# Performance work log

Measured on AMD Instinct MI355X. Metric: run time of the kernel, lower is better.

## Reference

```python
import jax, jax.numpy as jnp
import numpy as np

B, C, H, W = 8, 1, 256, 256
ALPHA, GAMMA = 0.25, 2.0
DICE_W, BOUNDARY_W, FOCAL_W = 1.0, 0.5, 1.0
EPS = 1e-06


def _dt1d(f, axis):
    # exact 1D squared-distance transform: out[i] = min_j (i-j)^2 + f[j]
    n = f.shape[axis]
    f = jnp.moveaxis(f, axis, -1)
    i = jnp.arange(n)
    D = ((i[:, None] - i[None, :]) ** 2).astype(f.dtype)  # [n, n]
    out = jnp.min(f[..., None, :] + D, axis=-1)
    return jnp.moveaxis(out, -1, axis)


def edt(mask):
    # Euclidean distance from nonzero elements to nearest zero element,
    # computed over ALL axes (matches scipy.distance_transform_edt on the 4D array).
    inf = jnp.asarray(float(sum(n * n for n in mask.shape) + 1), jnp.float32)
    f = jnp.where(mask, inf, jnp.float32(0.0))
    for ax in range(mask.ndim):  # structural loop over 4 axes
        f = _dt1d(f, ax)
    return jnp.sqrt(f)


def setup_inputs() -> dict:
    key = jax.random.key(0)
    k1, k2 = jax.random.split(key)
    logits = jax.random.normal(k1, (B, C, H, W), dtype=jnp.float32)
    targets = jax.random.uniform(k2, (B, C, H, W), dtype=jnp.float32)
    return {"logits": logits, "targets": targets}


def reference(logits, targets):
    p = jax.nn.sigmoid(logits)

    # Dice loss
    inter = jnp.sum(p * targets)
    dice = 1.0 - (2.0 * inter + EPS) / (jnp.sum(p) + jnp.sum(targets) + EPS)

    # Boundary loss (distance transform over the full 4D mask)
    dm = edt(targets > 0.5)
    boundary = jnp.mean(dm * (1.0 - p) ** 2)

    # Focal loss (stable BCE with logits)
    ce = jnp.maximum(logits, 0.0) - logits * targets + jnp.log1p(jnp.exp(-jnp.abs(logits)))
    p_t = p * targets + (1.0 - p) * (1.0 - targets)
    focal = jnp.mean(ALPHA * (1.0 - p_t) ** GAMMA * ce)

    return DICE_W * dice + BOUNDARY_W * boundary + FOCAL_W * focal
```

## Files before the change

kernel.cpp:

```cpp
#include <hip/hip_runtime.h>
#include <math.h>

namespace {

constexpr int Bn = 8;
constexpr int Hn = 256;
constexpr int Wn = 256;
constexpr int HW = Hn * Wn;
constexpr int Ntot = Bn * HW;
constexpr float INF_F = 131138.0f;
constexpr float EPSv = 1e-6f;

__device__ __forceinline__ float blkred(float v, float* sm) {
    #pragma unroll
    for (int o = 32; o > 0; o >>= 1) v += __shfl_down(v, o, 64);
    int lane = threadIdx.x & 63, wid = threadIdx.x >> 6;
    __syncthreads();
    if (lane == 0) sm[wid] = v;
    __syncthreads();
    return sm[0] + sm[1] + sm[2] + sm[3];
}

__device__ __forceinline__ void dt_wave4(const float* __restrict__ u,
                                         int lane, float res[4]) {
    const float4* u4 = reinterpret_cast<const float4*>(u);
    float fi[4], mA[4], mB[4];
    #pragma unroll
    for (int r = 0; r < 4; ++r) {
        fi[r] = (float)(4 * lane + r);
        mA[r] = 3.0e38f; mB[r] = 3.0e38f;
    }
    #pragma unroll 8
    for (int q = 0; q < 64; ++q) {
        float4 uu = u4[q];
        float j0 = (float)(-2 * (4 * q + 0));
        float j1 = (float)(-2 * (4 * q + 1));
        float j2 = (float)(-2 * (4 * q + 2));
        float j3 = (float)(-2 * (4 * q + 3));
        #pragma unroll
        for (int r = 0; r < 4; ++r) {
            mA[r] = fminf(fminf(mA[r], fmaf(j0, fi[r], uu.x)),
                          fmaf(j1, fi[r], uu.y));
            mB[r] = fminf(fminf(mB[r], fmaf(j2, fi[r], uu.z)),
                          fmaf(j3, fi[r], uu.w));
        }
    }
    #pragma unroll
    for (int r = 0; r < 4; ++r)
        res[r] = fminf(mA[r], mB[r]) + fi[r] * fi[r];
}

__global__ __launch_bounds__(256) void kA(const float* __restrict__ lg,
                                          const float* __restrict__ tg,
                                          float* __restrict__ f1,
                                          float* __restrict__ sq,
                                          float* __restrict__ pa) {
    int t = blockIdx.x * 256 + threadIdx.x;
    float sp = 0.f, st = 0.f, spt = 0.f, fo = 0.f;
    float fv[Bn];
    #pragma unroll
    for (int b = 0; b < Bn; b++) {
        float x  = lg[b * HW + t];
        float tv = tg[b * HW + t];
        float p  = 1.f / (1.f + expf(-x));
        sp  += p;
        st  += tv;
        spt += p * tv;
        float ce = fmaxf(x, 0.f) - x * tv + log1pf(expf(-fabsf(x)));
        float pt = p * tv + (1.f - p) * (1.f - tv);
        float om = 1.f - pt;
        fo += 0.25f * om * om * ce;
        float qn = 1.f - p;
        sq[b * HW + t] = qn * qn;
        fv[b] = (tv > 0.5f) ? INF_F : 0.f;
    }
    #pragma unroll
    for (int i = 0; i < Bn; i++) {
        float m = fv[0] + (float)(i * i);
        #pragma unroll
        for (int j = 1; j < Bn; j++) {
            int d = i - j;
            m = fminf(m, fv[j] + (float)(d * d));
        }
        f1[i * HW + t] = m;
    }
    __shared__ float sm[4];
    sp  = blkred(sp, sm);
    st  = blkred(st, sm);
    spt = blkred(spt, sm);
    fo  = blkred(fo, sm);
    if (threadIdx.x == 0) {
        float* o = pa + blockIdx.x * 4;
        o[0] = sp; o[1] = st; o[2] = spt; o[3] = fo;
    }
}

__global__ __launch_bounds__(256) void kW(const float* __restrict__ f1,
                                          float* __restrict__ g) {
    __shared__ __align__(16) float u[4][Wn];
    int wv = threadIdx.x >> 6, lane = threadIdx.x & 63;
    int line = blockIdx.x * 4 + wv;
    float4 v = reinterpret_cast<const float4*>(f1 + (size_t)line * Wn)[lane];
    float j0 = (float)(4 * lane);
    v.x += j0 * j0;
    v.y += (j0 + 1.f) * (j0 + 1.f);
    v.z += (j0 + 2.f) * (j0 + 2.f);
    v.w += (j0 + 3.f) * (j0 + 3.f);
    reinterpret_cast<float4*>(u[wv])[lane] = v;
    __syncthreads();
    float res[4];
    dt_wave4(u[wv], lane, res);
    float4 o = make_float4(res[0], res[1], res[2], res[3]);
    reinterpret_cast<float4*>(g + (size_t)line * Wn)[lane] = o;
}

__global__ __launch_bounds__(256) void kT(const float* __restrict__ g,
                                          const float* __restrict__ sq,
                                          float* __restrict__ gT,
                                          float* __restrict__ sqT) {
    int bid = blockIdx.x;
    int b  = bid >> 6;
    int ty = (bid >> 3) & 7;
    int tx = bid & 7;
    __shared__ float t0[32][33];
    __shared__ float t1[32][33];
    int c  = threadIdx.x & 31;
    int r0 = threadIdx.x >> 5;
    const float* gb = g  + (size_t)b * HW;
    const float* sb = sq + (size_t)b * HW;
    #pragma unroll
    for (int k = 0; k < 4; ++k) {
        int r = r0 + 8 * k;
        t0[r][c] = gb[(ty * 32 + r) * Wn + tx * 32 + c];
        t1[r][c] = sb[(ty * 32 + r) * Wn + tx * 32 + c];
    }
    __syncthreads();
    float* gTb = gT  + (size_t)b * HW;
    float* sTb = sqT + (size_t)b * HW;
    #pragma unroll
    for (int k = 0; k < 4; ++k) {
        int r = r0 + 8 * k;
        gTb[(tx * 32 + r) * Hn + ty * 32 + c] = t0[c][r];
        sTb[(tx * 32 + r) * Hn + ty * 32 + c] = t1[c][r];
    }
}

__global__ __launch_bounds__(256) void kH(const float* __restrict__ gT,
                                          const float* __restrict__ sqT,
                                          float* __restrict__ bp) {
    __shared__ __align__(16) float u[4][Hn];
    __shared__ float sm[4];
    int wv = threadIdx.x >> 6, lane = threadIdx.x & 63;
    int line = blockIdx.x * 4 + wv;
    float4 v = reinterpret_cast<const float4*>(gT + (size_t)line * Hn)[lane];
    float j0 = (float)(4 * lane);
    v.x += j0 * j0;
    v.y += (j0 + 1.f) * (j0 + 1.f);
    v.z += (j0 + 2.f) * (j0 + 2.f);
    v.w += (j0 + 3.f) * (j0 + 3.f);
    reinterpret_cast<float4*>(u[wv])[lane] = v;
    float4 sv = reinterpret_cast<const float4*>(sqT + (size_t)line * Hn)[lane];
    __syncthreads();
    float res[4];
    dt_wave4(u[wv], lane, res);
    float acc = sqrtf(res[0]) * sv.x + sqrtf(res[1]) * sv.y
              + sqrtf(res[2]) * sv.z + sqrtf(res[3]) * sv.w;
    acc = blkred(acc, sm);
    if (threadIdx.x == 0) bp[blockIdx.x] = acc;
}

__global__ __launch_bounds__(256) void kD(const float* __restrict__ pa,
                                          const float* __restrict__ bp,
                                          float* __restrict__ out) {
    __shared__ float sm[4];
    int t = threadIdx.x;
    float sp  = pa[t * 4 + 0];
    float st  = pa[t * 4 + 1];
    float spt = pa[t * 4 + 2];
    float fo  = pa[t * 4 + 3];
    float bs  = bp[t] + bp[t + 256];
    sp  = blkred(sp, sm);
    st  = blkred(st, sm);
    spt = blkred(spt, sm);
    fo  = blkred(fo, sm);
    bs  = blkred(bs, sm);
    if (t == 0) {
        float dice = 1.f - (2.f * spt + EPSv) / (sp + st + EPSv);
        float boundary = bs / (float)Ntot;
        float focal = fo / (float)Ntot;
        out[0] = 1.0f * dice + 0.5f * boundary + 1.0f * focal;
    }
}

}

extern "C" void kernel_launch(void* const* d_in, const int* in_sizes, int n_in,
                              void* d_out, int out_size, void* d_ws, size_t ws_size,
                              hipStream_t stream) {
    const float* lg = (const float*)d_in[0];
    const float* tg = (const float*)d_in[1];
    float* ws  = (float*)d_ws;
    float* f1  = ws;
    float* g   = ws + Ntot;
    float* sq  = ws + 2 * Ntot;
    float* gT  = ws + 3 * Ntot;
    float* sqT = ws + 4 * Ntot;
    float* pa  = ws + 5 * Ntot;
    float* bp  = ws + 5 * Ntot + 1024;

    kA<<<HW / 256, 256, 0, stream>>>(lg, tg, f1, sq, pa);
    kW<<<Bn * Hn / 4, 256, 0, stream>>>(f1, g);
    kT<<<Bn * 64, 256, 0, stream>>>(g, sq, gT, sqT);
    kH<<<Bn * Wn / 4, 256, 0, stream>>>(gT, sqT, bp);
    kD<<<1, 256, 0, stream>>>(pa, bp, (float*)d_out);
}
```

Baseline: 33.43 us.

## Fuse transpose into column DT pass and fold final reduction via last-block atomic

```diff
diff --git a/kernel.cpp b/kernel.cpp
--- a/kernel.cpp
+++ b/kernel.cpp
@@ -53,8 +53,9 @@
 __global__ __launch_bounds__(256) void kA(const float* __restrict__ lg,
                                           const float* __restrict__ tg,
                                           float* __restrict__ f1,
-                                          float* __restrict__ sq,
-                                          float* __restrict__ pa) {
+                                          float* __restrict__ pa,
+                                          unsigned int* __restrict__ cnt) {
+    if (blockIdx.x == 0 && threadIdx.x == 0) *cnt = 0u;
     int t = blockIdx.x * 256 + threadIdx.x;
     float sp = 0.f, st = 0.f, spt = 0.f, fo = 0.f;
     float fv[Bn];
@@ -70,8 +71,6 @@
         float pt = p * tv + (1.f - p) * (1.f - tv);
         float om = 1.f - pt;
         fo += 0.25f * om * om * ce;
-        float qn = 1.f - p;
-        sq[b * HW + t] = qn * qn;
         fv[b] = (tv > 0.5f) ? INF_F : 0.f;
     }
     #pragma unroll
@@ -114,81 +113,66 @@
     reinterpret_cast<float4*>(g + (size_t)line * Wn)[lane] = o;
 }
 
-__global__ __launch_bounds__(256) void kT(const float* __restrict__ g,
-                                          const float* __restrict__ sq,
-                                          float* __restrict__ gT,
-                                          float* __restrict__ sqT) {
-    int bid = blockIdx.x;
-    int b  = bid >> 6;
-    int ty = (bid >> 3) & 7;
-    int tx = bid & 7;
-    __shared__ float t0[32][33];
-    __shared__ float t1[32][33];
-    int c  = threadIdx.x & 31;
-    int r0 = threadIdx.x >> 5;
-    const float* gb = g  + (size_t)b * HW;
-    const float* sb = sq + (size_t)b * HW;
-    #pragma unroll
-    for (int k = 0; k < 4; ++k) {
-        int r = r0 + 8 * k;
-        t0[r][c] = gb[(ty * 32 + r) * Wn + tx * 32 + c];
-        t1[r][c] = sb[(ty * 32 + r) * Wn + tx * 32 + c];
-    }
-    __syncthreads();
-    float* gTb = gT  + (size_t)b * HW;
-    float* sTb = sqT + (size_t)b * HW;
-    #pragma unroll
-    for (int k = 0; k < 4; ++k) {
-        int r = r0 + 8 * k;
-        gTb[(tx * 32 + r) * Hn + ty * 32 + c] = t0[c][r];
-        sTb[(tx * 32 + r) * Hn + ty * 32 + c] = t1[c][r];
-    }
-}
-
-__global__ __launch_bounds__(256) void kH(const float* __restrict__ gT,
-                                          const float* __restrict__ sqT,
-                                          float* __restrict__ bp) {
+__global__ __launch_bounds__(256) void kH(const float* __restrict__ g,
+                                          const float* __restrict__ lg,
+                                          const float* __restrict__ pa,
+                                          float* __restrict__ bp,
+                                          unsigned int* __restrict__ cnt,
+                                          float* __restrict__ out,
+                                          int nblocks) {
     __shared__ __align__(16) float u[4][Hn];
+    __shared__ __align__(16) float xs[4][Hn];
     __shared__ float sm[4];
-    int wv = threadIdx.x >> 6, lane = threadIdx.x & 63;
-    int line = blockIdx.x * 4 + wv;
-    float4 v = reinterpret_cast<const float4*>(gT + (size_t)line * Hn)[lane];
-    float j0 = (float)(4 * lane);
-    v.x += j0 * j0;
-    v.y += (j0 + 1.f) * (j0 + 1.f);
-    v.z += (j0 + 2.f) * (j0 + 2.f);
-    v.w += (j0 + 3.f) * (j0 + 3.f);
-    reinterpret_cast<float4*>(u[wv])[lane] = v;
-    float4 sv = reinterpret_cast<const float4*>(sqT + (size_t)line * Hn)[lane];
+    __shared__ unsigned int tick;
+    int tid = threadIdx.x;
+    int wv = tid >> 6, lane = tid & 63;
+    int b  = blockIdx.x >> 6;
+    int w0 = (blockIdx.x & 63) * 4;
+    const float* gb = g  + (size_t)b * HW + w0;
+    const float* lb = lg + (size_t)b * HW + w0;
+    float4 gv = *reinterpret_cast<const float4*>(gb + (size_t)tid * Wn);
+    float4 xv = *reinterpret_cast<const float4*>(lb + (size_t)tid * Wn);
+    float h2 = (float)tid * (float)tid;
+    u[0][tid] = gv.x + h2; u[1][tid] = gv.y + h2;
+    u[2][tid] = gv.z + h2; u[3][tid] = gv.w + h2;
+    xs[0][tid] = xv.x; xs[1][tid] = xv.y; xs[2][tid] = xv.z; xs[3][tid] = xv.w;
     __syncthreads();
     float res[4];
     dt_wave4(u[wv], lane, res);
-    float acc = sqrtf(res[0]) * sv.x + sqrtf(res[1]) * sv.y
-              + sqrtf(res[2]) * sv.z + sqrtf(res[3]) * sv.w;
+    float acc = 0.f;
+    #pragma unroll
+    for (int r = 0; r < 4; ++r) {
+        int i = 4 * lane + r;
+        float x = xs[wv][i];
+        float s = 1.f / (1.f + expf(x));
+        acc += sqrtf(res[r]) * s * s;
+    }
     acc = blkred(acc, sm);
-    if (threadIdx.x == 0) bp[blockIdx.x] = acc;
-}
-
-__global__ __launch_bounds__(256) void kD(const float* __restrict__ pa,
-                                          const float* __restrict__ bp,
-                                          float* __restrict__ out) {
-    __shared__ float sm[4];
-    int t = threadIdx.x;
-    float sp  = pa[t * 4 + 0];
-    float st  = pa[t * 4 + 1];
-    float spt = pa[t * 4 + 2];
-    float fo  = pa[t * 4 + 3];
-    float bs  = bp[t] + bp[t + 256];
-    sp  = blkred(sp, sm);
-    st  = blkred(st, sm);
-    spt = blkred(spt, sm);
-    fo  = blkred(fo, sm);
-    bs  = blkred(bs, sm);
-    if (t == 0) {
-        float dice = 1.f - (2.f * spt + EPSv) / (sp + st + EPSv);
-        float boundary = bs / (float)Ntot;
-        float focal = fo / (float)Ntot;
-        out[0] = 1.0f * dice + 0.5f * boundary + 1.0f * focal;
+    if (tid == 0) {
+        bp[blockIdx.x] = acc;
+        __threadfence();
+        tick = atomicAdd(cnt, 1u);
+    }
+    __syncthreads();
+    if (tick == (unsigned int)(nblocks - 1)) {
+        __threadfence();
+        float sp  = pa[tid * 4 + 0];
+        float st  = pa[tid * 4 + 1];
+        float spt = pa[tid * 4 + 2];
+        float fo  = pa[tid * 4 + 3];
+        float bs  = bp[tid] + bp[tid + 256];
+        sp  = blkred(sp, sm);
+        st  = blkred(st, sm);
+        spt = blkred(spt, sm);
+        fo  = blkred(fo, sm);
+        bs  = blkred(bs, sm);
+        if (tid == 0) {
+            float dice = 1.f - (2.f * spt + EPSv) / (sp + st + EPSv);
+            float boundary = bs / (float)Ntot;
+            float focal = fo / (float)Ntot;
+            out[0] = 1.0f * dice + 0.5f * boundary + 1.0f * focal;
+            *cnt = 0u;
+        }
     }
 }
 
@@ -199,18 +183,15 @@
                               hipStream_t stream) {
     const float* lg = (const float*)d_in[0];
     const float* tg = (const float*)d_in[1];
-    float* ws  = (float*)d_ws;
-    float* f1  = ws;
-    float* g   = ws + Ntot;
-    float* sq  = ws + 2 * Ntot;
-    float* gT  = ws + 3 * Ntot;
-    float* sqT = ws + 4 * Ntot;
-    float* pa  = ws + 5 * Ntot;
-    float* bp  = ws + 5 * Ntot + 1024;
+    float* ws = (float*)d_ws;
+    float* f1 = ws;
+    float* g  = ws + Ntot;
+    float* pa = ws + 2 * Ntot;
+    float* bp = ws + 2 * Ntot + 1024;
+    unsigned int* cnt = (unsigned int*)(ws + 2 * Ntot + 2048);
 
-    kA<<<HW / 256, 256, 0, stream>>>(lg, tg, f1, sq, pa);
+    kA<<<HW / 256, 256, 0, stream>>>(lg, tg, f1, pa, cnt);
     kW<<<Bn * Hn / 4, 256, 0, stream>>>(f1, g);
-    kT<<<Bn * 64, 256, 0, stream>>>(g, sq, gT, sqT);
-    kH<<<Bn * Wn / 4, 256, 0, stream>>>(gT, sqT, bp);
-    kD<<<1, 256, 0, stream>>>(pa, bp, (float*)d_out);
+    kH<<<Bn * Wn / 4, 256, 0, stream>>>(g, lg, pa, bp, cnt, (float*)d_out,
+                                        Bn * Wn / 4);
 }
```

Measured after the change: 39.37 us. 1.18x slower.

## Recompute (1-p)^2 from logits in column pass instead of storing and transposing it

Applied to the files above, without the earlier changes.

```diff
diff --git a/kernel.cpp b/kernel.cpp
--- a/kernel.cpp
+++ b/kernel.cpp
@@ -24,25 +24,25 @@
 __device__ __forceinline__ void dt_wave4(const float* __restrict__ u,
                                          int lane, float res[4]) {
     const float4* u4 = reinterpret_cast<const float4*>(u);
-    float fi[4], mA[4], mB[4];
+    float fi[4], ni2[4], mA[4], mB[4];
     #pragma unroll
     for (int r = 0; r < 4; ++r) {
-        fi[r] = (float)(4 * lane + r);
+        fi[r]  = (float)(4 * lane + r);
+        ni2[r] = -2.0f * fi[r];
         mA[r] = 3.0e38f; mB[r] = 3.0e38f;
     }
+    float jb = 0.f;
     #pragma unroll 8
     for (int q = 0; q < 64; ++q) {
         float4 uu = u4[q];
-        float j0 = (float)(-2 * (4 * q + 0));
-        float j1 = (float)(-2 * (4 * q + 1));
-        float j2 = (float)(-2 * (4 * q + 2));
-        float j3 = (float)(-2 * (4 * q + 3));
+        float j0 = jb, j1 = jb + 1.f, j2 = jb + 2.f, j3 = jb + 3.f;
+        jb += 4.f;
         #pragma unroll
         for (int r = 0; r < 4; ++r) {
-            mA[r] = fminf(fminf(mA[r], fmaf(j0, fi[r], uu.x)),
-                          fmaf(j1, fi[r], uu.y));
-            mB[r] = fminf(fminf(mB[r], fmaf(j2, fi[r], uu.z)),
-                          fmaf(j3, fi[r], uu.w));
+            mA[r] = fminf(fminf(mA[r], fmaf(ni2[r], j0, uu.x)),
+                          fmaf(ni2[r], j1, uu.y));
+            mB[r] = fminf(fminf(mB[r], fmaf(ni2[r], j2, uu.z)),
+                          fmaf(ni2[r], j3, uu.w));
         }
     }
     #pragma unroll
@@ -53,7 +53,6 @@
 __global__ __launch_bounds__(256) void kA(const float* __restrict__ lg,
                                           const float* __restrict__ tg,
                                           float* __restrict__ f1,
-                                          float* __restrict__ sq,
                                           float* __restrict__ pa) {
     int t = blockIdx.x * 256 + threadIdx.x;
     float sp = 0.f, st = 0.f, spt = 0.f, fo = 0.f;
@@ -70,8 +69,6 @@
         float pt = p * tv + (1.f - p) * (1.f - tv);
         float om = 1.f - pt;
         fo += 0.25f * om * om * ce;
-        float qn = 1.f - p;
-        sq[b * HW + t] = qn * qn;
         fv[b] = (tv > 0.5f) ? INF_F : 0.f;
     }
     #pragma unroll
@@ -110,48 +107,42 @@
     __syncthreads();
     float res[4];
     dt_wave4(u[wv], lane, res);
-    float4 o = make_float4(res[0], res[1], res[2], res[3]);
-    reinterpret_cast<float4*>(g + (size_t)line * Wn)[lane] = o;
+    reinterpret_cast<float4*>(g + (size_t)line * Wn)[lane] =
+        make_float4(res[0], res[1], res[2], res[3]);
 }
 
 __global__ __launch_bounds__(256) void kT(const float* __restrict__ g,
-                                          const float* __restrict__ sq,
-                                          float* __restrict__ gT,
-                                          float* __restrict__ sqT) {
+                                          float* __restrict__ gT) {
     int bid = blockIdx.x;
     int b  = bid >> 6;
     int ty = (bid >> 3) & 7;
     int tx = bid & 7;
-    __shared__ float t0[32][33];
-    __shared__ float t1[32][33];
+    __shared__ float t[32][33];
     int c  = threadIdx.x & 31;
     int r0 = threadIdx.x >> 5;
-    const float* gb = g  + (size_t)b * HW;
-    const float* sb = sq + (size_t)b * HW;
+    const float* gb = g + (size_t)b * HW;
     #pragma unroll
     for (int k = 0; k < 4; ++k) {
         int r = r0 + 8 * k;
-        t0[r][c] = gb[(ty * 32 + r) * Wn + tx * 32 + c];
-        t1[r][c] = sb[(ty * 32 + r) * Wn + tx * 32 + c];
-    }
-    __syncthreads();
-    float* gTb = gT  + (size_t)b * HW;
-    float* sTb = sqT + (size_t)b * HW;
+        t[r][c] = gb[(ty * 32 + r) * Wn + tx * 32 + c];
+    }
+    __syncthreads();
+    float* gTb = gT + (size_t)b * HW;
     #pragma unroll
     for (int k = 0; k < 4; ++k) {
         int r = r0 + 8 * k;
-        gTb[(tx * 32 + r) * Hn + ty * 32 + c] = t0[c][r];
-        sTb[(tx * 32 + r) * Hn + ty * 32 + c] = t1[c][r];
+        gTb[(tx * 32 + r) * Hn + ty * 32 + c] = t[c][r];
     }
 }
 
 __global__ __launch_bounds__(256) void kH(const float* __restrict__ gT,
-                                          const float* __restrict__ sqT,
+                                          const float* __restrict__ lg,
                                           float* __restrict__ bp) {
     __shared__ __align__(16) float u[4][Hn];
     __shared__ float sm[4];
     int wv = threadIdx.x >> 6, lane = threadIdx.x & 63;
     int line = blockIdx.x * 4 + wv;
+    int b = line >> 8, w = line & 255;
     float4 v = reinterpret_cast<const float4*>(gT + (size_t)line * Hn)[lane];
     float j0 = (float)(4 * lane);
     v.x += j0 * j0;
@@ -159,12 +150,20 @@
     v.z += (j0 + 2.f) * (j0 + 2.f);
     v.w += (j0 + 3.f) * (j0 + 3.f);
     reinterpret_cast<float4*>(u[wv])[lane] = v;
-    float4 sv = reinterpret_cast<const float4*>(sqT + (size_t)line * Hn)[lane];
+    const float* lb = lg + (size_t)b * HW + w;
+    float xv[4];
+    #pragma unroll
+    for (int r = 0; r < 4; ++r)
+        xv[r] = lb[(size_t)(4 * lane + r) * Wn];
     __syncthreads();
     float res[4];
     dt_wave4(u[wv], lane, res);
-    float acc = sqrtf(res[0]) * sv.x + sqrtf(res[1]) * sv.y
-              + sqrtf(res[2]) * sv.z + sqrtf(res[3]) * sv.w;
+    float acc = 0.f;
+    #pragma unroll
+    for (int r = 0; r < 4; ++r) {
+        float s = 1.f / (1.f + expf(xv[r]));
+        acc += sqrtf(res[r]) * s * s;
+    }
     acc = blkred(acc, sm);
     if (threadIdx.x == 0) bp[blockIdx.x] = acc;
 }
@@ -199,18 +198,16 @@
                               hipStream_t stream) {
     const float* lg = (const float*)d_in[0];
     const float* tg = (const float*)d_in[1];
-    float* ws  = (float*)d_ws;
-    float* f1  = ws;
-    float* g   = ws + Ntot;
-    float* sq  = ws + 2 * Ntot;
-    float* gT  = ws + 3 * Ntot;
-    float* sqT = ws + 4 * Ntot;
-    float* pa  = ws + 5 * Ntot;
-    float* bp  = ws + 5 * Ntot + 1024;
-
-    kA<<<HW / 256, 256, 0, stream>>>(lg, tg, f1, sq, pa);
+    float* ws = (float*)d_ws;
+    float* f1 = ws;
+    float* g  = ws + Ntot;
+    float* gT = ws + 2 * Ntot;
+    float* pa = ws + 3 * Ntot;
+    float* bp = ws + 3 * Ntot + 1024;
+
+    kA<<<HW / 256, 256, 0, stream>>>(lg, tg, f1, pa);
     kW<<<Bn * Hn / 4, 256, 0, stream>>>(f1, g);
-    kT<<<Bn * 64, 256, 0, stream>>>(g, sq, gT, sqT);
-    kH<<<Bn * Wn / 4, 256, 0, stream>>>(gT, sqT, bp);
+    kT<<<Bn * 64, 256, 0, stream>>>(g, gT);
+    kH<<<Bn * Wn / 4, 256, 0, stream>>>(gT, lg, bp);
     kD<<<1, 256, 0, stream>>>(pa, bp, (float*)d_out);
 }
```

Result: faster. 30.78 us (-7.9%).
